# Kernel optimization log

Hardware: AMD Instinct MI355X
Metric: run time of the kernel (lower is better)

The kernel has to match this reference:

```python
import jax, jax.numpy as jnp
import numpy as np

HEADS = 4
DIM_HEAD = 32
SCALE = DIM_HEAD ** -0.5


def setup_inputs() -> dict:
    key = jax.random.key(0)
    k1, k2, k3 = jax.random.split(key, 3)
    dim = 128
    hidden = HEADS * DIM_HEAD  # 128
    x = jax.random.normal(k1, (4, dim, 64, 64), dtype=jnp.float32)
    w_qkv = jax.random.normal(k2, (3 * hidden, dim), dtype=jnp.float32) * (dim ** -0.5)
    w_out = jax.random.normal(k3, (dim, hidden), dtype=jnp.float32) * (hidden ** -0.5)
    b_out = jnp.zeros((dim,), dtype=jnp.float32)
    return {"x": x, "w_qkv": w_qkv, "w_out": w_out, "b_out": b_out}


def reference(x, w_qkv, w_out, b_out):
    b, c, h, w = x.shape
    n = h * w
    # 1x1 conv == channel matmul per pixel
    qkv = jnp.einsum('oc,bchw->bohw', w_qkv, x)  # [b, 3*hidden, h, w]
    q, k, v = jnp.split(qkv, 3, axis=1)
    # b (heads d) x y -> b heads d (x y)
    def to_heads(t):
        return t.reshape(b, HEADS, DIM_HEAD, n)
    q = to_heads(q) * SCALE
    k = to_heads(k)
    v = to_heads(v)
    sim = jnp.einsum('bhdi,bhdj->bhij', q, k)          # [b, heads, n, n]
    attn = jax.nn.softmax(sim, axis=-1)
    out = jnp.einsum('bhij,bhdj->bhid', attn, v)        # [b, heads, n, d]
    # b h (x y) d -> b (h d) x y
    out = out.transpose(0, 1, 3, 2).reshape(b, HEADS * DIM_HEAD, h, w)
    out = jnp.einsum('oc,bchw->bohw', w_out, out) + b_out[None, :, None, None]
    return out
```

## Files before the change

kernel.cpp:

```cpp
#include <hip/hip_runtime.h>
#include <math.h>

#define NHEAD 4
#define DHEAD 32
#define NPIX  4096
#define CIN   128
#define RP    4

typedef __bf16 bf16_t;
typedef __bf16 bf16x8 __attribute__((ext_vector_type(8)));
typedef __bf16 bf16x4 __attribute__((ext_vector_type(4)));
typedef float  f32x4  __attribute__((ext_vector_type(4)));

constexpr float QSCALE = 0.17677669529663687f * 1.4426950408889634f;

__global__ void __launch_bounds__(256) qkv_mfma(
    const float* __restrict__ x, const float* __restrict__ wqkv,
    ushort* __restrict__ qb, ushort* __restrict__ kb, ushort* __restrict__ vT) {
  __shared__ ushort Xls[32 * 136];
  const int blk = blockIdx.x, tid = threadIdx.x;
  const int half = blockIdx.y;
  const int wave = tid >> 6, lane = tid & 63;
  const int n = lane & 15, quad = lane >> 4;
  const int bb = blk >> 7;
  const int p0 = (blk & 127) * 32;

  {
    const int pc = tid & 7, c0 = (tid >> 3) * 4;
    const float* xp = x + ((size_t)bb * CIN + c0) * NPIX + p0 + pc * 4;
    float4 r0 = *(const float4*)xp;
    float4 r1 = *(const float4*)(xp + NPIX);
    float4 r2 = *(const float4*)(xp + 2 * NPIX);
    float4 r3 = *(const float4*)(xp + 3 * NPIX);
    bf16x4 w0 = {(bf16_t)r0.x, (bf16_t)r1.x, (bf16_t)r2.x, (bf16_t)r3.x};
    bf16x4 w1 = {(bf16_t)r0.y, (bf16_t)r1.y, (bf16_t)r2.y, (bf16_t)r3.y};
    bf16x4 w2 = {(bf16_t)r0.z, (bf16_t)r1.z, (bf16_t)r2.z, (bf16_t)r3.z};
    bf16x4 w3 = {(bf16_t)r0.w, (bf16_t)r1.w, (bf16_t)r2.w, (bf16_t)r3.w};
    *(bf16x4*)&Xls[(pc * 4 + 0) * 136 + c0] = w0;
    *(bf16x4*)&Xls[(pc * 4 + 1) * 136 + c0] = w1;
    *(bf16x4*)&Xls[(pc * 4 + 2) * 136 + c0] = w2;
    *(bf16x4*)&Xls[(pc * 4 + 3) * 136 + c0] = w3;
  }
  __syncthreads();

  bf16x8 xf[2][4];
#pragma unroll
  for (int nt = 0; nt < 2; ++nt)
#pragma unroll
    for (int k = 0; k < 4; ++k)
      xf[nt][k] = *(const bf16x8*)&Xls[(nt * 16 + n) * 136 + k * 32 + quad * 8];

#pragma unroll
  for (int mt = 0; mt < 3; ++mt) {
    const int ot = half * 12 + wave * 3 + mt;
    const int type = ot >> 3;
    const int wt = ot & 7, head = wt >> 1, d0 = (wt & 1) * 16;
    const int bh = bb * NHEAD + head;
    const float sc = (type == 0) ? QSCALE : 1.f;
    bf16x8 wf4[4];
#pragma unroll
    for (int k = 0; k < 4; ++k) {
      const float* ws = wqkv + (size_t)(ot * 16 + n) * CIN + k * 32 + quad * 8;
      float4 a = *(const float4*)ws;
      float4 b = *(const float4*)(ws + 4);
      wf4[k] = (bf16x8){(bf16_t)(a.x * sc), (bf16_t)(a.y * sc),
                        (bf16_t)(a.z * sc), (bf16_t)(a.w * sc),
                        (bf16_t)(b.x * sc), (bf16_t)(b.y * sc),
                        (bf16_t)(b.z * sc), (bf16_t)(b.w * sc)};
    }
    f32x4 acc[2] = {{0.f, 0.f, 0.f, 0.f}, {0.f, 0.f, 0.f, 0.f}};
    if (type < 2) {
#pragma unroll
      for (int k = 0; k < 4; ++k)
#pragma unroll
        for (int nt = 0; nt < 2; ++nt)
          acc[nt] = __builtin_amdgcn_mfma_f32_16x16x32_bf16(wf4[k], xf[nt][k], acc[nt], 0, 0, 0);
      ushort* dst = (type == 0) ? qb : kb;
#pragma unroll
      for (int nt = 0; nt < 2; ++nt) {
        bf16x4 o = {(bf16_t)acc[nt][0], (bf16_t)acc[nt][1],
                    (bf16_t)acc[nt][2], (bf16_t)acc[nt][3]};
        *(bf16x4*)(dst + ((size_t)bh * NPIX + p0 + nt * 16 + n) * DHEAD + d0 + quad * 4) = o;
      }
    } else {
#pragma unroll
      for (int k = 0; k < 4; ++k)
#pragma unroll
        for (int nt = 0; nt < 2; ++nt)
          acc[nt] = __builtin_amdgcn_mfma_f32_16x16x32_bf16(xf[nt][k], wf4[k], acc[nt], 0, 0, 0);
#pragma unroll
      for (int nt = 0; nt < 2; ++nt) {
        bf16x4 o = {(bf16_t)acc[nt][0], (bf16_t)acc[nt][1],
                    (bf16_t)acc[nt][2], (bf16_t)acc[nt][3]};
        *(bf16x4*)(vT + ((size_t)bh * DHEAD + d0 + n) * NPIX + p0 + nt * 16 + quad * 4) = o;
      }
    }
  }
}

__device__ __forceinline__ void ft_load(const ushort* kb0, const ushort* vb0,
                                        int t, bf16x8* kf, bf16x8* vf) {
#pragma unroll
  for (int p = 0; p < 2; ++p) {
#pragma unroll
    for (int s = 0; s < 2; ++s)
      kf[p * 2 + s] = *(const bf16x8*)(kb0 + (size_t)(t * 64 + p * 32 + s * 4) * DHEAD);
#pragma unroll
    for (int dp = 0; dp < 2; ++dp)
      vf[p * 2 + dp] = *(const bf16x8*)(vb0 + (size_t)dp * 16 * NPIX + t * 64 + p * 32);
  }
}

__device__ __forceinline__ void ft_compute(const bf16x8* qf, const bf16x8* kf,
                                           const bf16x8* vf, const bf16x8 ones,
                                           f32x4 O[RP][2], f32x4* Ol) {
  const f32x4 zero = {0.f, 0.f, 0.f, 0.f};
  __builtin_amdgcn_s_setprio(1);
#pragma unroll
  for (int p = 0; p < 2; ++p) {
#pragma unroll
    for (int rp = 0; rp < RP; ++rp) {
      f32x4 sa = __builtin_amdgcn_mfma_f32_16x16x32_bf16(kf[p * 2 + 0], qf[rp], zero, 0, 0, 0);
      f32x4 sb = __builtin_amdgcn_mfma_f32_16x16x32_bf16(kf[p * 2 + 1], qf[rp], zero, 0, 0, 0);
      bf16x8 pf;
#pragma unroll
      for (int r = 0; r < 4; ++r) {
        pf[r]     = (bf16_t)__builtin_amdgcn_exp2f(sa[r]);
        pf[r + 4] = (bf16_t)__builtin_amdgcn_exp2f(sb[r]);
      }
      O[rp][0] = __builtin_amdgcn_mfma_f32_16x16x32_bf16(pf, vf[p * 2 + 0], O[rp][0], 0, 0, 0);
      O[rp][1] = __builtin_amdgcn_mfma_f32_16x16x32_bf16(pf, vf[p * 2 + 1], O[rp][1], 0, 0, 0);
      Ol[rp]   = __builtin_amdgcn_mfma_f32_16x16x32_bf16(pf, ones, Ol[rp], 0, 0, 0);
    }
  }
  __builtin_amdgcn_s_setprio(0);
}

__global__ void __launch_bounds__(256, 2) flash_mfma(
    const ushort* __restrict__ qb, const ushort* __restrict__ kbuf,
    const ushort* __restrict__ vTb, float* __restrict__ part) {
  const int tid = threadIdx.x, wave = tid >> 6, lane = tid & 63;
  const int n = lane & 15, quad = lane >> 4;

  const int id = blockIdx.x;
  const int g  = (id & 7) | ((id >> 7) << 3);
  const int qbk = (id >> 3) & 15;
  const int bh = g >> 2;
  const int js = g & 3;
  const int qrel = qbk * 256 + wave * 64;

  const ushort* kg = kbuf + (size_t)bh * NPIX * DHEAD;
  const ushort* vg = vTb + (size_t)bh * DHEAD * NPIX;

  bf16x8 qf[RP];
#pragma unroll
  for (int rp = 0; rp < RP; ++rp)
    qf[rp] = *(const bf16x8*)(qb +
        ((size_t)bh * NPIX + qrel + rp * 16 + n) * DHEAD + quad * 8);

  f32x4 O[RP][2], Ol[RP];
#pragma unroll
  for (int rp = 0; rp < RP; ++rp) {
    O[rp][0] = (f32x4){0.f, 0.f, 0.f, 0.f};
    O[rp][1] = (f32x4){0.f, 0.f, 0.f, 0.f};
    Ol[rp]   = (f32x4){0.f, 0.f, 0.f, 0.f};
  }
  const bf16_t one = (bf16_t)1.0f;
  const bf16x8 ones = {one, one, one, one, one, one, one, one};

  const int pk = ((n >> 2) << 3) | (n & 3);
  const ushort* kb0 = kg + (size_t)(js * 1024 + pk) * DHEAD + quad * 8;
  const ushort* vb0 = vg + (size_t)n * NPIX + js * 1024 + quad * 8;

  bf16x8 kA[4], vA[4], kB[4], vB[4];
  ft_load(kb0, vb0, 0, kA, vA);
#pragma unroll 1
  for (int t = 0; t < 16; t += 2) {
    ft_load(kb0, vb0, t + 1, kB, vB);
    ft_compute(qf, kA, vA, ones, O, Ol);
    if (t + 2 < 16) ft_load(kb0, vb0, t + 2, kA, vA);
    ft_compute(qf, kB, vB, ones, O, Ol);
  }

  float* pb = part + ((size_t)js * 65536 + (size_t)bh * NPIX + qrel) * 36;
#pragma unroll
  for (int rp = 0; rp < RP; ++rp)
#pragma unroll
    for (int r = 0; r < 4; ++r) {
      const int q = rp * 16 + quad * 4 + r;
      pb[(size_t)q * 36 + n]      = O[rp][0][r];
      pb[(size_t)q * 36 + 16 + n] = O[rp][1][r];
      if (n == 0) pb[(size_t)q * 36 + 32] = Ol[rp][r];
    }
}

__global__ void __launch_bounds__(256) out_fused(
    const float* __restrict__ part, const float* __restrict__ wout,
    const float* __restrict__ bias, float* __restrict__ out) {
  __shared__ ushort AOls[16 * 136];
  const int blk = blockIdx.x, tid = threadIdx.x;
  const int wave = tid >> 6, lane = tid & 63;
  const int n = lane & 15, quad = lane >> 4;
  const int bb = blk >> 8;
  const int p0 = (blk & 255) * 16;
  const int oc0 = wave * 32;

  bf16x8 wf[2][4];
#pragma unroll
  for (int mt = 0; mt < 2; ++mt)
#pragma unroll
    for (int k = 0; k < 4; ++k) {
      const float* ws = wout + (size_t)((wave * 2 + mt) * 16 + n) * CIN + k * 32 + quad * 8;
      float4 a = *(const float4*)ws;
      float4 b = *(const float4*)(ws + 4);
      wf[mt][k] = (bf16x8){(bf16_t)a.x, (bf16_t)a.y, (bf16_t)a.z, (bf16_t)a.w,
                           (bf16_t)b.x, (bf16_t)b.y, (bf16_t)b.z, (bf16_t)b.w};
    }

  {
    const int px = tid >> 4, c16 = tid & 15;
    const int h = c16 >> 2, doff = (c16 & 3) * 8;
    const size_t rowbase = (size_t)(bb * NHEAD + h) * NPIX + p0 + px;
    float s[8];
#pragma unroll
    for (int e = 0; e < 8; ++e) s[e] = 0.f;
    float l = 0.f;
#pragma unroll
    for (int js = 0; js < 4; ++js) {
      const float* pp = part + ((size_t)js * 65536 + rowbase) * 36;
      f32x4 a0 = *(const f32x4*)(pp + doff);
      f32x4 a1 = *(const f32x4*)(pp + doff + 4);
#pragma unroll
      for (int e = 0; e < 4; ++e) {
        s[e]     += a0[e];
        s[4 + e] += a1[e];
      }
      l += pp[32];
    }
    const float inv = 1.f / l;
    bf16x8 o0;
#pragma unroll
    for (int e = 0; e < 8; ++e) o0[e] = (bf16_t)(s[e] * inv);
    *(bf16x8*)&AOls[px * 136 + c16 * 8] = o0;
  }
  __syncthreads();

  bf16x8 bfr[4];
#pragma unroll
  for (int k = 0; k < 4; ++k)
    bfr[k] = *(const bf16x8*)&AOls[n * 136 + k * 32 + quad * 8];

  f32x4 acc[2];
#pragma unroll
  for (int mt = 0; mt < 2; ++mt) acc[mt] = (f32x4){0.f, 0.f, 0.f, 0.f};
#pragma unroll
  for (int k = 0; k < 4; ++k)
#pragma unroll
    for (int mt = 0; mt < 2; ++mt)
      acc[mt] = __builtin_amdgcn_mfma_f32_16x16x32_bf16(
          wf[mt][k], bfr[k], acc[mt], 0, 0, 0);

#pragma unroll
  for (int mt = 0; mt < 2; ++mt) {
    const int oc = oc0 + mt * 16 + quad * 4;
#pragma unroll
    for (int r = 0; r < 4; ++r)
      out[((size_t)bb * CIN + oc + r) * NPIX + p0 + n] =
          acc[mt][r] + bias[oc + r];
  }
}

extern "C" void kernel_launch(void* const* d_in, const int* in_sizes, int n_in,
                              void* d_out, int out_size, void* d_ws, size_t ws_size,
                              hipStream_t stream) {
  const float* x     = (const float*)d_in[0];
  const float* w_qkv = (const float*)d_in[1];
  const float* w_out = (const float*)d_in[2];
  const float* b_out = (const float*)d_in[3];
  float* out = (float*)d_out;

  char* base = (char*)d_ws;
  ushort* qb   = (ushort*)base;
  ushort* kb   = (ushort*)(base + (size_t)4 * 1024 * 1024);
  ushort* vT   = (ushort*)(base + (size_t)8 * 1024 * 1024);
  float*  part = (float*)(base + (size_t)12 * 1024 * 1024);

  qkv_mfma<<<dim3(512, 2), 256, 0, stream>>>(x, w_qkv, qb, kb, vT);
  flash_mfma<<<dim3(1024), 256, 0, stream>>>(qb, kb, vT, part);
  out_fused<<<dim3(1024), 256, 0, stream>>>(part, w_out, b_out, out);
}
```

Baseline: 145.4 us.

## Double query rows per wave and split keys eight ways in flash kernel

Each wave now holds 128 query rows (RP 8) instead of 64, so every K/V fragment loaded from memory is reused across twice as many MFMA tiles. To keep enough blocks in flight, the key dimension is split into 8 slices when the workspace is large enough, otherwise 4. The out kernel reduces over a runtime number of partial results. This raises register pressure, since the O accumulators double, and adds partial-sum traffic when 8 splits are used.

```diff
diff --git a/kernel.cpp b/kernel.cpp
--- a/kernel.cpp
+++ b/kernel.cpp
@@ -5,7 +5,7 @@
 #define DHEAD 32
 #define NPIX  4096
 #define CIN   128
-#define RP    4
+#define RP    8
 
 typedef __bf16 bf16_t;
 typedef __bf16 bf16x8 __attribute__((ext_vector_type(8)));
@@ -136,18 +136,21 @@
   __builtin_amdgcn_s_setprio(0);
 }
 
+template <int JSC>
 __global__ void __launch_bounds__(256, 2) flash_mfma(
     const ushort* __restrict__ qb, const ushort* __restrict__ kbuf,
     const ushort* __restrict__ vTb, float* __restrict__ part) {
+  constexpr int KSL = NPIX / JSC;
+  constexpr int NT  = KSL / 64;
   const int tid = threadIdx.x, wave = tid >> 6, lane = tid & 63;
   const int n = lane & 15, quad = lane >> 4;
 
   const int id = blockIdx.x;
-  const int g  = (id & 7) | ((id >> 7) << 3);
-  const int qbk = (id >> 3) & 15;
-  const int bh = g >> 2;
-  const int js = g & 3;
-  const int qrel = qbk * 256 + wave * 64;
+  const int g  = (id & 7) | ((id >> 6) << 3);
+  const int qbk = (id >> 3) & 7;
+  const int bh = g / JSC;
+  const int js = g % JSC;
+  const int qrel = qbk * 512 + wave * 128;
 
   const ushort* kg = kbuf + (size_t)bh * NPIX * DHEAD;
   const ushort* vg = vTb + (size_t)bh * DHEAD * NPIX;
@@ -169,16 +172,16 @@
   const bf16x8 ones = {one, one, one, one, one, one, one, one};
 
   const int pk = ((n >> 2) << 3) | (n & 3);
-  const ushort* kb0 = kg + (size_t)(js * 1024 + pk) * DHEAD + quad * 8;
-  const ushort* vb0 = vg + (size_t)n * NPIX + js * 1024 + quad * 8;
+  const ushort* kb0 = kg + (size_t)(js * KSL + pk) * DHEAD + quad * 8;
+  const ushort* vb0 = vg + (size_t)n * NPIX + js * KSL + quad * 8;
 
   bf16x8 kA[4], vA[4], kB[4], vB[4];
   ft_load(kb0, vb0, 0, kA, vA);
 #pragma unroll 1
-  for (int t = 0; t < 16; t += 2) {
+  for (int t = 0; t < NT; t += 2) {
     ft_load(kb0, vb0, t + 1, kB, vB);
     ft_compute(qf, kA, vA, ones, O, Ol);
-    if (t + 2 < 16) ft_load(kb0, vb0, t + 2, kA, vA);
+    if (t + 2 < NT) ft_load(kb0, vb0, t + 2, kA, vA);
     ft_compute(qf, kB, vB, ones, O, Ol);
   }
 
@@ -196,7 +199,7 @@
 
 __global__ void __launch_bounds__(256) out_fused(
     const float* __restrict__ part, const float* __restrict__ wout,
-    const float* __restrict__ bias, float* __restrict__ out) {
+    const float* __restrict__ bias, float* __restrict__ out, int jsc) {
   __shared__ ushort AOls[16 * 136];
   const int blk = blockIdx.x, tid = threadIdx.x;
   const int wave = tid >> 6, lane = tid & 63;
@@ -225,8 +228,8 @@
 #pragma unroll
     for (int e = 0; e < 8; ++e) s[e] = 0.f;
     float l = 0.f;
-#pragma unroll
-    for (int js = 0; js < 4; ++js) {
+#pragma unroll 4
+    for (int js = 0; js < jsc; ++js) {
       const float* pp = part + ((size_t)js * 65536 + rowbase) * 36;
       f32x4 a0 = *(const f32x4*)(pp + doff);
       f32x4 a1 = *(const f32x4*)(pp + doff + 4);
@@ -285,7 +288,14 @@
   ushort* vT   = (ushort*)(base + (size_t)8 * 1024 * 1024);
   float*  part = (float*)(base + (size_t)12 * 1024 * 1024);
 
+  const size_t need8 = (size_t)12 * 1024 * 1024 +
+                       (size_t)8 * 65536 * 36 * sizeof(float);
+  const int jsc = (ws_size >= need8) ? 8 : 4;
+
   qkv_mfma<<<dim3(512, 2), 256, 0, stream>>>(x, w_qkv, qb, kb, vT);
-  flash_mfma<<<dim3(1024), 256, 0, stream>>>(qb, kb, vT, part);
-  out_fused<<<dim3(1024), 256, 0, stream>>>(part, w_out, b_out, out);
-}
+  if (jsc == 8)
+    flash_mfma<8><<<dim3(1024), 256, 0, stream>>>(qb, kb, vT, part);
+  else
+    flash_mfma<4><<<dim3(512), 256, 0, stream>>>(qb, kb, vT, part);
+  out_fused<<<dim3(1024), 256, 0, stream>>>(part, w_out, b_out, out, jsc);
+}
```

Result: faster. 142.4 us (-2.0%).

## Split keys across waves and reduce flash partials in LDS, emit bf16

Applied to the files above, without the earlier changes.

The flash kernel now gives each wave a quarter of the keys for the same 128 query rows, instead of spreading the key split across separate blocks. Each wave doubles its query rows per thread (RP=8). The four partial O/l results are combined in shared memory, normalized in-kernel and written as bf16. The output projection then reads the attention output directly, with no cross-split reduction. This removes the large fp32 partial buffer round trip through global memory, at the cost of much more LDS per block, higher register pressure and fewer blocks.

```diff
diff --git a/kernel.cpp b/kernel.cpp
--- a/kernel.cpp
+++ b/kernel.cpp
@@ -5,7 +5,7 @@
 #define DHEAD 32
 #define NPIX  4096
 #define CIN   128
-#define RP    4
+#define RP    8
 
 typedef __bf16 bf16_t;
 typedef __bf16 bf16x8 __attribute__((ext_vector_type(8)));
@@ -138,16 +138,16 @@
 
 __global__ void __launch_bounds__(256, 2) flash_mfma(
     const ushort* __restrict__ qb, const ushort* __restrict__ kbuf,
-    const ushort* __restrict__ vTb, float* __restrict__ part) {
+    const ushort* __restrict__ vTb, ushort* __restrict__ ao) {
+  __shared__ float Ols[4 * 128 * 36];
   const int tid = threadIdx.x, wave = tid >> 6, lane = tid & 63;
   const int n = lane & 15, quad = lane >> 4;
 
   const int id = blockIdx.x;
-  const int g  = (id & 7) | ((id >> 7) << 3);
-  const int qbk = (id >> 3) & 15;
-  const int bh = g >> 2;
-  const int js = g & 3;
-  const int qrel = qbk * 256 + wave * 64;
+  const int bh = id & 15;
+  const int qblk = id >> 4;
+  const int js = wave;
+  const int qrel = qblk * 128;
 
   const ushort* kg = kbuf + (size_t)bh * NPIX * DHEAD;
   const ushort* vg = vTb + (size_t)bh * DHEAD * NPIX;
@@ -182,22 +182,52 @@
     ft_compute(qf, kB, vB, ones, O, Ol);
   }
 
-  float* pb = part + ((size_t)js * 65536 + (size_t)bh * NPIX + qrel) * 36;
-#pragma unroll
-  for (int rp = 0; rp < RP; ++rp)
-#pragma unroll
-    for (int r = 0; r < 4; ++r) {
-      const int q = rp * 16 + quad * 4 + r;
-      pb[(size_t)q * 36 + n]      = O[rp][0][r];
-      pb[(size_t)q * 36 + 16 + n] = O[rp][1][r];
-      if (n == 0) pb[(size_t)q * 36 + 32] = Ol[rp][r];
-    }
+  {
+    float* pb = &Ols[wave * 128 * 36];
+#pragma unroll
+    for (int rp = 0; rp < RP; ++rp)
+#pragma unroll
+      for (int r = 0; r < 4; ++r) {
+        const int q = rp * 16 + quad * 4 + r;
+        pb[q * 36 + n]      = O[rp][0][r];
+        pb[q * 36 + 16 + n] = O[rp][1][r];
+        if (n == 0) pb[q * 36 + 32] = Ol[rp][r];
+      }
+  }
+  __syncthreads();
+
+  {
+    const int q = tid >> 1, dh = tid & 1;
+    f32x4 A0 = {0.f, 0.f, 0.f, 0.f}, A1 = A0, A2 = A0, A3 = A0;
+    float l = 0.f;
+#pragma unroll
+    for (int w = 0; w < 4; ++w) {
+      const float* pp = &Ols[(w * 128 + q) * 36 + dh * 16];
+      A0 += *(const f32x4*)pp;
+      A1 += *(const f32x4*)(pp + 4);
+      A2 += *(const f32x4*)(pp + 8);
+      A3 += *(const f32x4*)(pp + 12);
+      l += pp[32 - dh * 16];
+    }
+    const float inv = 1.f / l;
+    bf16x8 o0, o1;
+#pragma unroll
+    for (int e = 0; e < 4; ++e) {
+      o0[e]     = (bf16_t)(A0[e] * inv);
+      o0[e + 4] = (bf16_t)(A1[e] * inv);
+      o1[e]     = (bf16_t)(A2[e] * inv);
+      o1[e + 4] = (bf16_t)(A3[e] * inv);
+    }
+    ushort* dst = ao + ((size_t)((bh >> 2) * NPIX + qrel + q) * CIN
+                        + (bh & 3) * 32 + dh * 16);
+    *(bf16x8*)dst = o0;
+    *(bf16x8*)(dst + 8) = o1;
+  }
 }
 
 __global__ void __launch_bounds__(256) out_fused(
-    const float* __restrict__ part, const float* __restrict__ wout,
+    const ushort* __restrict__ ao, const float* __restrict__ wout,
     const float* __restrict__ bias, float* __restrict__ out) {
-  __shared__ ushort AOls[16 * 136];
   const int blk = blockIdx.x, tid = threadIdx.x;
   const int wave = tid >> 6, lane = tid & 63;
   const int n = lane & 15, quad = lane >> 4;
@@ -217,38 +247,11 @@
                            (bf16_t)b.x, (bf16_t)b.y, (bf16_t)b.z, (bf16_t)b.w};
     }
 
-  {
-    const int px = tid >> 4, c16 = tid & 15;
-    const int h = c16 >> 2, doff = (c16 & 3) * 8;
-    const size_t rowbase = (size_t)(bb * NHEAD + h) * NPIX + p0 + px;
-    float s[8];
-#pragma unroll
-    for (int e = 0; e < 8; ++e) s[e] = 0.f;
-    float l = 0.f;
-#pragma unroll
-    for (int js = 0; js < 4; ++js) {
-      const float* pp = part + ((size_t)js * 65536 + rowbase) * 36;
-      f32x4 a0 = *(const f32x4*)(pp + doff);
-      f32x4 a1 = *(const f32x4*)(pp + doff + 4);
-#pragma unroll
-      for (int e = 0; e < 4; ++e) {
-        s[e]     += a0[e];
-        s[4 + e] += a1[e];
-      }
-      l += pp[32];
-    }
-    const float inv = 1.f / l;
-    bf16x8 o0;
-#pragma unroll
-    for (int e = 0; e < 8; ++e) o0[e] = (bf16_t)(s[e] * inv);
-    *(bf16x8*)&AOls[px * 136 + c16 * 8] = o0;
-  }
-  __syncthreads();
-
   bf16x8 bfr[4];
 #pragma unroll
   for (int k = 0; k < 4; ++k)
-    bfr[k] = *(const bf16x8*)&AOls[n * 136 + k * 32 + quad * 8];
+    bfr[k] = *(const bf16x8*)(ao +
+        ((size_t)(bb * NPIX + p0 + n) * CIN + k * 32 + quad * 8));
 
   f32x4 acc[2];
 #pragma unroll
@@ -280,12 +283,12 @@
   float* out = (float*)d_out;
 
   char* base = (char*)d_ws;
-  ushort* qb   = (ushort*)base;
-  ushort* kb   = (ushort*)(base + (size_t)4 * 1024 * 1024);
-  ushort* vT   = (ushort*)(base + (size_t)8 * 1024 * 1024);
-  float*  part = (float*)(base + (size_t)12 * 1024 * 1024);
+  ushort* qb = (ushort*)base;
+  ushort* kb = (ushort*)(base + (size_t)4 * 1024 * 1024);
+  ushort* vT = (ushort*)(base + (size_t)8 * 1024 * 1024);
+  ushort* ao = (ushort*)(base + (size_t)12 * 1024 * 1024);
 
   qkv_mfma<<<dim3(512, 2), 256, 0, stream>>>(x, w_qkv, qb, kb, vT);
-  flash_mfma<<<dim3(1024), 256, 0, stream>>>(qb, kb, vT, part);
-  out_fused<<<dim3(1024), 256, 0, stream>>>(part, w_out, b_out, out);
-}
+  flash_mfma<<<dim3(512), 256, 0, stream>>>(qb, kb, vT, ao);
+  out_fused<<<dim3(1024), 256, 0, stream>>>(ao, w_out, b_out, out);
+}
```

Result: faster. 131.0 us (median of 2 runs) (-9.9%).
